# Performance work log

Hardware: AMD Instinct MI355X
Metric: run time of the kernel (lower is better)

## Reference

```python
import jax, jax.numpy as jnp
import numpy as np

B = 16384
R, N_NODES, K, N_LAYERS, LATENT = 5, 68, 32, 3, 68


def setup_inputs() -> dict:
    key = jax.random.key(0)
    ks = jax.random.split(key, 6)
    z = jax.random.normal(ks[0], (B, LATENT), dtype=jnp.float32)
    adjacency = jax.random.randint(ks[1], (N_NODES, K), 0, N_NODES)
    # init_fc weights stored as [latent, n_nodes] so forward is z @ fc_w[r] + fc_b[r]
    fc_w = jax.random.normal(ks[2], (R, LATENT, N_NODES), dtype=jnp.float32) * 0.1
    fc_b = jax.random.normal(ks[3], (R, N_NODES), dtype=jnp.float32) * 0.1
    gcn_w = jax.random.normal(ks[4], (R, N_LAYERS, N_NODES, K), dtype=jnp.float32) * 0.1
    gcn_b = jax.random.normal(ks[5], (R, N_LAYERS, N_NODES), dtype=jnp.float32) * 0.1
    return {"z": z, "adjacency": adjacency, "fc_w": fc_w, "fc_b": fc_b,
            "gcn_w": gcn_w, "gcn_b": gcn_b}


def _gcn_layer(x, adjacency, w, b):
    # x: [B, N]; adjacency: [N, K] int; w: [N, K]; b: [N]
    x_nb = x[:, adjacency]                      # [B, N, K] ragged-style gather
    val = jnp.einsum('bnk,nk->bn', x_nb, w) + b  # per-node weighted neighbor sum
    return jax.nn.sigmoid(val)


def reference(z, adjacency, fc_w, fc_b, gcn_w, gcn_b):
    b = z.shape[0]
    sc_sum = jnp.zeros((b, N_NODES, N_NODES), dtype=z.dtype)
    for r in range(R):
        x = z @ fc_w[r] + fc_b[r]               # init_fc[r]
        for l in range(N_LAYERS):
            x = _gcn_layer(x, adjacency, gcn_w[r, l], gcn_b[r, l])
        # rank-1 outer product per sample: bmm(x.unsqueeze(2), x.unsqueeze(1))
        sc_sum = sc_sum + x[:, :, None] * x[:, None, :]
    sc_sum = 0.5 * (sc_sum + jnp.swapaxes(sc_sum, 1, 2))
    return sc_sum.reshape(b, -1)
```

## Files before the change

kernel.cpp:

```cpp
#include <hip/hip_runtime.h>
#include <math.h>

#define R_ 5
#define NN 68
#define KK 32
#define NL 3
#define LAT 68
#define NSL 17
#define ROWQ (NN / 4)
#define NF4 ((NN * NN) / 4)
#define BBK2 16
#define LSTR 344

__global__ __launch_bounds__(128) void densify_k(
    const int* __restrict__ adj, const float* __restrict__ gw,
    float* __restrict__ wd) {
  const int rl = blockIdx.x;
  const int t = threadIdx.x;
  __shared__ float col[NN][NN + 4];
  for (int i = t; i < NN * (NN + 4); i += 128) (&col[0][0])[i] = 0.0f;
  __syncthreads();
  if (t < NN) {
    const int n = t;
    const int* ar = adj + n * KK;
    const float* wr = gw + ((size_t)rl * NN + n) * KK;
    for (int k = 0; k < KK; ++k) col[ar[k]][n] += wr[k];
  }
  __syncthreads();
  float* wout = wd + (size_t)rl * NN * NN;
  for (int i = t; i < NN * NN; i += 128) {
    const int m = i / NN, n = i - m * NN;
    wout[i] = col[m][n];
  }
}

__global__ __launch_bounds__(256) void ztr_k(const float* __restrict__ z,
                                             float* __restrict__ zT, int B) {
  const int t = threadIdx.x;
  const int b0 = blockIdx.x * 64;
  __shared__ float zls[64][LAT + 1];
  for (int idx = t; idx < 64 * ROWQ; idx += 256) {
    const int row = idx / ROWQ, q = idx - row * ROWQ;
    const float4 v =
        *reinterpret_cast<const float4*>(z + (size_t)(b0 + row) * LAT + 4 * q);
    zls[row][4 * q + 0] = v.x;
    zls[row][4 * q + 1] = v.y;
    zls[row][4 * q + 2] = v.z;
    zls[row][4 * q + 3] = v.w;
  }
  __syncthreads();
  for (int idx = t; idx < LAT * 64; idx += 256) {
    const int l = idx >> 6, bb = idx & 63;
    zT[(size_t)l * B + b0 + bb] = zls[bb][l];
  }
}

__global__ __launch_bounds__(256) void chain_k(
    const float* __restrict__ zT, const float* __restrict__ fc_w,
    const float* __restrict__ fc_b, const float* __restrict__ wd,
    const float* __restrict__ gb, float* __restrict__ X, int B, int nb) {
  const int t = threadIdx.x;
  const int lane = t & 63;
  const int w = __builtin_amdgcn_readfirstlane(t >> 6);
  const int n0 = w * NSL;
  const int r = blockIdx.x / nb;
  const int b0 = (blockIdx.x - r * nb) * 64;

  __shared__ float xs[NN][64];

  for (int idx = t; idx < NN * 64; idx += 256) {
    const int m = idx >> 6;
    xs[m][idx & 63] = zT[(size_t)m * B + b0 + (idx & 63)];
  }
  __syncthreads();

  float acc[NSL];

#pragma unroll 1
  for (int stage = 0; stage < 1 + NL; ++stage) {
    const float* wb = (stage == 0) ? fc_w + (size_t)r * LAT * NN
                                   : wd + (size_t)(r * NL + stage - 1) * NN * NN;
    const float* bias = (stage == 0) ? fc_b + r * NN
                                     : gb + (size_t)(r * NL + stage - 1) * NN;
#pragma unroll
    for (int j = 0; j < NSL; ++j) acc[j] = bias[n0 + j];

#pragma unroll 2
    for (int m = 0; m < NN; ++m) {
      const float xm = xs[m][lane];
      const float* wr = wb + m * NN + n0;
#pragma unroll
      for (int j = 0; j < NSL; ++j) acc[j] = fmaf(xm, wr[j], acc[j]);
    }
    if (stage > 0) {
#pragma unroll
      for (int j = 0; j < NSL; ++j)
        acc[j] = 1.0f / (1.0f + __expf(-acc[j]));
    }
    if (stage < NL) {
      __syncthreads();
#pragma unroll
      for (int j = 0; j < NSL; ++j) xs[n0 + j][lane] = acc[j];
      __syncthreads();
    }
  }

  float* Xb = X + ((size_t)r * NN + n0) * B + b0 + lane;
#pragma unroll
  for (int j = 0; j < NSL; ++j) Xb[(size_t)j * B] = acc[j];
}

__global__ __launch_bounds__(256) void outer_k(const float* __restrict__ X,
                                               float* __restrict__ out, int B) {
  const int t = threadIdx.x;
  const int b0 = blockIdx.x * BBK2;
  __shared__ float xls[BBK2 * LSTR];

  for (int idx = t; idx < R_ * NN * BBK2; idx += 256) {
    const int rn = idx >> 4, bb = idx & (BBK2 - 1);
    xls[bb * LSTR + rn] = X[(size_t)rn * B + b0 + bb];
  }
  __syncthreads();

  float4* ob = reinterpret_cast<float4*>(out) + (size_t)b0 * NF4;
  const int total = BBK2 * NF4;
  for (int fg = t; fg < total; fg += 256) {
    const int bb = fg / NF4;
    const int f = fg - bb * NF4;
    const int i = f / ROWQ;
    const int q = f - i * ROWQ;
    const float* xb = &xls[bb * LSTR];
    float4 a = make_float4(0.f, 0.f, 0.f, 0.f);
#pragma unroll
    for (int r = 0; r < R_; ++r) {
      const float xi = xb[r * NN + i];
      const float4 xj = *reinterpret_cast<const float4*>(xb + r * NN + 4 * q);
      a.x = fmaf(xi, xj.x, a.x);
      a.y = fmaf(xi, xj.y, a.y);
      a.z = fmaf(xi, xj.z, a.z);
      a.w = fmaf(xi, xj.w, a.w);
    }
    ob[fg] = a;
  }
}

extern "C" void kernel_launch(void* const* d_in, const int* in_sizes, int n_in,
                              void* d_out, int out_size, void* d_ws, size_t ws_size,
                              hipStream_t stream) {
  const float* z    = (const float*)d_in[0];
  const int*   adj  = (const int*)  d_in[1];
  const float* fc_w = (const float*)d_in[2];
  const float* fc_b = (const float*)d_in[3];
  const float* gw   = (const float*)d_in[4];
  const float* gb   = (const float*)d_in[5];
  float* out = (float*)d_out;

  const int B = in_sizes[0] / LAT;
  float* wd = (float*)d_ws;
  float* zT = wd + R_ * NL * NN * NN;
  float* X  = zT + (size_t)LAT * B;

  const int nb = B / 64;

  densify_k<<<R_ * NL, 128, 0, stream>>>(adj, gw, wd);
  ztr_k<<<B / 64, 256, 0, stream>>>(z, zT, B);
  chain_k<<<R_ * nb, 256, 0, stream>>>(zT, fc_w, fc_b, wd, gb, X, B, nb);
  outer_k<<<B / BBK2, 256, 0, stream>>>(X, out, B);
}
```

Baseline: 139.8 us.

## Register-tile outer product in outer_k and use nontemporal output stores

The outer-product kernel now gives each thread one sample and one column quad, keeping the five column float4 vectors in registers. It loops over row groups, reusing those vectors across four rows each, and handles the leftover 17th column quad in a separate tail loop. All output writes become nontemporal stores to avoid polluting cache with the large write-only output. This cuts per-element index division and shared-memory loads, but the store pattern now strides across rows, which may reduce write coalescing.

```diff
diff --git a/kernel.cpp b/kernel.cpp
--- a/kernel.cpp
+++ b/kernel.cpp
@@ -12,6 +12,8 @@
 #define BBK2 16
 #define LSTR 344
 
+typedef float f32x4 __attribute__((ext_vector_type(4)));
+
 __global__ __launch_bounds__(128) void densify_k(
     const int* __restrict__ adj, const float* __restrict__ gw,
     float* __restrict__ wd) {
@@ -122,25 +124,57 @@
   }
   __syncthreads();
 
-  float4* ob = reinterpret_cast<float4*>(out) + (size_t)b0 * NF4;
-  const int total = BBK2 * NF4;
-  for (int fg = t; fg < total; fg += 256) {
-    const int bb = fg / NF4;
-    const int f = fg - bb * NF4;
-    const int i = f / ROWQ;
-    const int q = f - i * ROWQ;
-    const float* xb = &xls[bb * LSTR];
+  const int lane = t & 63;
+  const int wv = t >> 6;
+  const int bb = wv * 4 + (lane >> 4);
+  const int c  = lane & 15;
+  const float* xb = &xls[bb * LSTR];
+
+  float4 xj[R_];
+#pragma unroll
+  for (int r = 0; r < R_; ++r)
+    xj[r] = *reinterpret_cast<const float4*>(xb + r * NN + 4 * c);
+
+  f32x4* obase = reinterpret_cast<f32x4*>(out) + (size_t)(b0 + bb) * NF4 + c;
+#pragma unroll 2
+  for (int g = 0; g < 17; ++g) {
+    float4 xi[R_];
+#pragma unroll
+    for (int r = 0; r < R_; ++r)
+      xi[r] = *reinterpret_cast<const float4*>(xb + r * NN + 4 * g);
+#pragma unroll
+    for (int k = 0; k < 4; ++k) {
+      float4 a = make_float4(0.f, 0.f, 0.f, 0.f);
+#pragma unroll
+      for (int r = 0; r < R_; ++r) {
+        const float s = reinterpret_cast<const float*>(&xi[r])[k];
+        a.x = fmaf(s, xj[r].x, a.x);
+        a.y = fmaf(s, xj[r].y, a.y);
+        a.z = fmaf(s, xj[r].z, a.z);
+        a.w = fmaf(s, xj[r].w, a.w);
+      }
+      f32x4 av = {a.x, a.y, a.z, a.w};
+      __builtin_nontemporal_store(av, obase + (size_t)(4 * g + k) * ROWQ);
+    }
+  }
+
+  for (int fg = t; fg < BBK2 * NN; fg += 256) {
+    const int bb2 = fg / NN, i = fg - bb2 * NN;
+    const float* xb2 = &xls[bb2 * LSTR];
     float4 a = make_float4(0.f, 0.f, 0.f, 0.f);
 #pragma unroll
     for (int r = 0; r < R_; ++r) {
-      const float xi = xb[r * NN + i];
-      const float4 xj = *reinterpret_cast<const float4*>(xb + r * NN + 4 * q);
-      a.x = fmaf(xi, xj.x, a.x);
-      a.y = fmaf(xi, xj.y, a.y);
-      a.z = fmaf(xi, xj.z, a.z);
-      a.w = fmaf(xi, xj.w, a.w);
-    }
-    ob[fg] = a;
+      const float s = xb2[r * NN + i];
+      const float4 x4 = *reinterpret_cast<const float4*>(xb2 + r * NN + 64);
+      a.x = fmaf(s, x4.x, a.x);
+      a.y = fmaf(s, x4.y, a.y);
+      a.z = fmaf(s, x4.z, a.z);
+      a.w = fmaf(s, x4.w, a.w);
+    }
+    f32x4 av = {a.x, a.y, a.z, a.w};
+    __builtin_nontemporal_store(
+        av, reinterpret_cast<f32x4*>(out) + (size_t)(b0 + bb2) * NF4 +
+                (size_t)i * ROWQ + 16);
   }
 }
 
```

Result: slower. 286.8 us (+105.2%).
